# Kernel tuning notes

Hardware: AMD Instinct MI355X
Metric: run time of the kernel (lower is better)

The kernel has to match this reference:

```python
import jax, jax.numpy as jnp
import numpy as np

B = 4096
N = 4097  # num_samples; basis fit uses N-1 columns


def _trapz_cumsum(x, t):
    # y[..., 0] = 0; y[..., i] = y[..., i-1] + 0.5*(t[i]-t[i-1])*(x[..., i-1]+x[..., i])
    dt = t[1:] - t[:-1]                                   # (N-1,)
    inc = 0.5 * dt * (x[..., :-1] + x[..., 1:])           # (B,1,N-1)
    zero = jnp.zeros(x.shape[:-1] + (1,), x.dtype)
    return jnp.concatenate([zero, jnp.cumsum(inc, axis=-1)], axis=-1)  # (B,1,N)


def setup_inputs() -> dict:
    key = jax.random.key(0)
    k1, k2 = jax.random.split(key)
    # positive signal so ny + cumsum(x) stays > 0 (needed for pow/log)
    x = jax.random.uniform(k1, (B, 1, N), dtype=jnp.float32, minval=0.1, maxval=1.1)
    # strictly increasing time grid
    dt = jax.random.uniform(k2, (N,), dtype=jnp.float32, minval=1e-3, maxval=1e-2)
    t = jnp.cumsum(dt)
    params = jnp.array([0.5, 1.0], dtype=jnp.float32)  # [r, ny]
    return {"x": x, "t": t, "params": params}


def reference(x, t, params):
    r, ny = params[0], params[1]
    y = _trapz_cumsum(x, t)                  # (B,1,N)
    z = ny + y[:, 0, 1:]                     # (B,N-1)
    phi = jnp.stack([z, z ** r], axis=1)     # (B,2,N-1)  basis matrix
    phip = jnp.linalg.pinv(phi)              # (B,N-1,2)
    x_sl = x[:, :, 1:]                       # (B,1,N-1)
    coeffs = x_sl @ phip                     # (B,1,2)
    x_hat = coeffs @ phi                     # (B,1,N-1)
    res = x_sl - x_hat                       # (B,1,N-1)
    r2 = jnp.sum(res ** 2, axis=-1)          # (B,1)
    return coeffs, x_hat, res, r2
```

## Files before the change

### kernel.cpp

```cpp
#include <hip/hip_runtime.h>

typedef float f32x4 __attribute__((ext_vector_type(4)));

constexpr int NPTS = 4097;
constexpr int M    = 4096;
constexpr int TPB  = 256;
constexpr int NW   = TPB / 64;
constexpr int NJ   = 4;

struct Lds {
    float wt[NW][NJ];
    float gram[NW][5];
    float r2s[NW];
};

template<int S>
__device__ __forceinline__ void scan4(const f32x4 a, const f32x4 c,
                                      float d0, float d1, float d2, float d3,
                                      float (&xsj)[4], float (&zlj)[4], float& gsj)
{
    const float m[8] = {a.x, a.y, a.z, a.w, c.x, c.y, c.z, c.w};
    const float x0 = m[S+0], x1 = m[S+1], x2 = m[S+2], x3 = m[S+3], x4 = m[S+4];
    const float i0 = d0 * (x0 + x1);
    const float i1 = d1 * (x1 + x2);
    const float i2 = d2 * (x2 + x3);
    const float i3 = d3 * (x3 + x4);
    zlj[0] = i0;
    zlj[1] = i0 + i1;
    zlj[2] = zlj[1] + i2;
    zlj[3] = zlj[2] + i3;
    gsj = zlj[3];
    xsj[0] = x1; xsj[1] = x2; xsj[2] = x3; xsj[3] = x4;
}

template<int S, bool RHALF>
__device__ __forceinline__ void body(const float* __restrict__ x,
                                     const float* __restrict__ t,
                                     float r, float ny,
                                     float* __restrict__ out,
                                     int b, int B, Lds& L)
{
    const int tid  = threadIdx.x;
    const int lane = tid & 63;
    const int wid  = tid >> 6;

    const float* __restrict__ xal = x + (size_t)b * NPTS - S;

    float xs[NJ][4];
    float zl[NJ][4];
    float gs[NJ];

#pragma unroll
    for (int j = 0; j < NJ; ++j) {
        const int e = j * 1024 + tid * 4;
        const f32x4 a4 = *(const f32x4*)(xal + e);
        const f32x4 c4 = *(const f32x4*)(xal + e + 4);
        const f32x4 tq = *(const f32x4*)(t + e);
        float tn = __shfl_down(tq.x, 1, 64);
        if (lane == 63) tn = t[e + 4];
        const float d0 = 0.5f * (tq.y - tq.x);
        const float d1 = 0.5f * (tq.z - tq.y);
        const float d2 = 0.5f * (tq.w - tq.z);
        const float d3 = 0.5f * (tn   - tq.w);
        scan4<S>(a4, c4, d0, d1, d2, d3, xs[j], zl[j], gs[j]);
    }

    float sc[NJ];
#pragma unroll
    for (int c = 0; c < NJ; ++c) sc[c] = gs[c];
#pragma unroll
    for (int d = 1; d < 64; d <<= 1) {
#pragma unroll
        for (int c = 0; c < NJ; ++c) {
            float u = __shfl_up(sc[c], d, 64);
            if (lane >= d) sc[c] += u;
        }
    }
    if (lane == 63) {
#pragma unroll
        for (int c = 0; c < NJ; ++c) L.wt[wid][c] = sc[c];
    }
    __syncthreads();

    float woff[NJ] = {}, Tt[NJ] = {};
#pragma unroll
    for (int w = 0; w < NW; ++w) {
#pragma unroll
        for (int c = 0; c < NJ; ++c) {
            const float v = L.wt[w][c];
            Tt[c] += v;
            if (w < wid) woff[c] += v;
        }
    }
    float zb[NJ];
    {
        float jacc = 0.f;
#pragma unroll
        for (int j = 0; j < NJ; ++j) {
            zb[j] = ny + jacc + woff[j] + (sc[j] - gs[j]);
            jacc += Tt[j];
        }
    }

    float s0 = 0, s1 = 0, s2 = 0, s3 = 0, s4 = 0;
#pragma unroll
    for (int j = 0; j < NJ; ++j) {
        float pzz = 0, pzw = 0, pww = 0, pxz = 0, pxw = 0;
#pragma unroll
        for (int i = 0; i < 4; ++i) {
            const float z = zb[j] + zl[j][i];
            zl[j][i] = z;
            const float w = RHALF ? sqrtf(z) : powf(z, r);
            const float xv = xs[j][i];
            pzz = fmaf(z,  z, pzz);
            pzw = fmaf(z,  w, pzw);
            pww = fmaf(w,  w, pww);
            pxz = fmaf(xv, z, pxz);
            pxw = fmaf(xv, w, pxw);
        }
        s0 += pzz; s1 += pzw; s2 += pww; s3 += pxz; s4 += pxw;
    }
#pragma unroll
    for (int d = 32; d > 0; d >>= 1) {
        s0 += __shfl_down(s0, d, 64);
        s1 += __shfl_down(s1, d, 64);
        s2 += __shfl_down(s2, d, 64);
        s3 += __shfl_down(s3, d, 64);
        s4 += __shfl_down(s4, d, 64);
    }
    if (lane == 0) {
        L.gram[wid][0] = s0; L.gram[wid][1] = s1; L.gram[wid][2] = s2;
        L.gram[wid][3] = s3; L.gram[wid][4] = s4;
    }
    __syncthreads();

    double a0 = 0, a1 = 0, a2 = 0, a3 = 0, a4 = 0;
#pragma unroll
    for (int w = 0; w < NW; ++w) {
        a0 += L.gram[w][0]; a1 += L.gram[w][1]; a2 += L.gram[w][2];
        a3 += L.gram[w][3]; a4 += L.gram[w][4];
    }
    const double det = a0 * a2 - a1 * a1;
    const double inv = 1.0 / det;
    const float c0 = (float)((a3 * a2 - a4 * a1) * inv);
    const float c1 = (float)((a4 * a0 - a3 * a1) * inv);
    if (tid == 0) {
        out[(size_t)b * 2 + 0] = c0;
        out[(size_t)b * 2 + 1] = c1;
    }

    float* __restrict__ xhat = out + (size_t)B * 2 + (size_t)b * M;
    float* __restrict__ res  = xhat + (size_t)B * M;

    float r2 = 0.f;
#pragma unroll
    for (int j = 0; j < NJ; ++j) {
        const int e = j * 1024 + tid * 4;
        f32x4 hv, rv;
#pragma unroll
        for (int i = 0; i < 4; ++i) {
            const float z = zl[j][i];
            const float w = RHALF ? sqrtf(z) : powf(z, r);
            const float h  = c0 * z + c1 * w;
            const float ev = xs[j][i] - h;
            hv[i] = h; rv[i] = ev;
            r2 = fmaf(ev, ev, r2);
        }
        *(f32x4*)(xhat + e) = hv;
        *(f32x4*)(res  + e) = rv;
    }
#pragma unroll
    for (int d = 32; d > 0; d >>= 1) r2 += __shfl_down(r2, d, 64);
    if (lane == 0) L.r2s[wid] = r2;
    __syncthreads();
    if (tid == 0) {
        float acc = 0.f;
#pragma unroll
        for (int w = 0; w < NW; ++w) acc += L.r2s[w];
        out[(size_t)B * 2 + 2 * (size_t)B * M + b] = acc;
    }
}

__global__ __launch_bounds__(TPB)
void vp_kernel(const float* __restrict__ x, const float* __restrict__ t,
               const float* __restrict__ params, float* __restrict__ out, int B)
{
    __shared__ Lds L;
    const float r  = params[0];
    const float ny = params[1];
    const int  b   = blockIdx.x;

    if (r == 0.5f) {
        switch (b & 3) {
        case 0:  body<0, true>(x, t, r, ny, out, b, B, L); break;
        case 1:  body<1, true>(x, t, r, ny, out, b, B, L); break;
        case 2:  body<2, true>(x, t, r, ny, out, b, B, L); break;
        default: body<3, true>(x, t, r, ny, out, b, B, L); break;
        }
    } else {
        switch (b & 3) {
        case 0:  body<0, false>(x, t, r, ny, out, b, B, L); break;
        case 1:  body<1, false>(x, t, r, ny, out, b, B, L); break;
        case 2:  body<2, false>(x, t, r, ny, out, b, B, L); break;
        default: body<3, false>(x, t, r, ny, out, b, B, L); break;
        }
    }
}

extern "C" void kernel_launch(void* const* d_in, const int* in_sizes, int n_in,
                              void* d_out, int out_size, void* d_ws, size_t ws_size,
                              hipStream_t stream) {
    const float* x = (const float*)d_in[0];
    const float* t = (const float*)d_in[1];
    const float* p = (const float*)d_in[2];
    float* out     = (float*)d_out;
    const int B    = in_sizes[0] / NPTS;

    vp_kernel<<<dim3(B), dim3(TPB), 0, stream>>>(x, t, p, out, B);
}
```

Measured before the change: 41.29 us.

## Map one row per wavefront and recompute scan from global memory per pass

Each wavefront now processes a whole row instead of a 256-thread block per row, which removes all LDS traffic and block barriers. Rows are handled in 16 sequential chunks with a wave-level prefix scan that carries a running sum. Only the per-chunk base offsets are kept in registers; x and t are re-read from memory and the local scan is recomputed in the Gram and output passes. This trades extra loads (mostly cache hits) and a serial per-chunk scan for lower register pressure and more resident waves via launch_bounds occupancy 8. Grid size assumes B is divisible by 4.

Measured after the change: 70.03 us. +69.6%, slower.

```diff
diff --git a/kernel.cpp b/kernel.cpp
--- a/kernel.cpp
+++ b/kernel.cpp
@@ -5,113 +5,80 @@
 constexpr int NPTS = 4097;
 constexpr int M    = 4096;
 constexpr int TPB  = 256;
-constexpr int NW   = TPB / 64;
-constexpr int NJ   = 4;
-
-struct Lds {
-    float wt[NW][NJ];
-    float gram[NW][5];
-    float r2s[NW];
-};
+constexpr int WPB  = 4;
+constexpr int NG   = 16;
 
 template<int S>
-__device__ __forceinline__ void scan4(const f32x4 a, const f32x4 c,
-                                      float d0, float d1, float d2, float d3,
-                                      float (&xsj)[4], float (&zlj)[4], float& gsj)
+__device__ __forceinline__ void group_u(const f32x4 a, const f32x4 c,
+                                        const f32x4 tq, float tn,
+                                        float (&u)[4], float (&xsj)[4])
 {
     const float m[8] = {a.x, a.y, a.z, a.w, c.x, c.y, c.z, c.w};
     const float x0 = m[S+0], x1 = m[S+1], x2 = m[S+2], x3 = m[S+3], x4 = m[S+4];
+    const float d0 = 0.5f * (tq.y - tq.x);
+    const float d1 = 0.5f * (tq.z - tq.y);
+    const float d2 = 0.5f * (tq.w - tq.z);
+    const float d3 = 0.5f * (tn   - tq.w);
     const float i0 = d0 * (x0 + x1);
     const float i1 = d1 * (x1 + x2);
     const float i2 = d2 * (x2 + x3);
     const float i3 = d3 * (x3 + x4);
-    zlj[0] = i0;
-    zlj[1] = i0 + i1;
-    zlj[2] = zlj[1] + i2;
-    zlj[3] = zlj[2] + i3;
-    gsj = zlj[3];
+    u[0] = i0;
+    u[1] = i0 + i1;
+    u[2] = u[1] + i2;
+    u[3] = u[2] + i3;
     xsj[0] = x1; xsj[1] = x2; xsj[2] = x3; xsj[3] = x4;
 }
 
 template<int S, bool RHALF>
-__device__ __forceinline__ void body(const float* __restrict__ x,
-                                     const float* __restrict__ t,
-                                     float r, float ny,
-                                     float* __restrict__ out,
-                                     int b, int B, Lds& L)
+__device__ __forceinline__ void wave_body(
+    const float* __restrict__ x, const float* __restrict__ t,
+    float r, float ny, float* __restrict__ out, int b, int B)
 {
-    const int tid  = threadIdx.x;
-    const int lane = tid & 63;
-    const int wid  = tid >> 6;
-
+    const int lane = threadIdx.x & 63;
     const float* __restrict__ xal = x + (size_t)b * NPTS - S;
 
-    float xs[NJ][4];
-    float zl[NJ][4];
-    float gs[NJ];
-
-#pragma unroll
-    for (int j = 0; j < NJ; ++j) {
-        const int e = j * 1024 + tid * 4;
-        const f32x4 a4 = *(const f32x4*)(xal + e);
-        const f32x4 c4 = *(const f32x4*)(xal + e + 4);
-        const f32x4 tq = *(const f32x4*)(t + e);
-        float tn = __shfl_down(tq.x, 1, 64);
-        if (lane == 63) tn = t[e + 4];
-        const float d0 = 0.5f * (tq.y - tq.x);
-        const float d1 = 0.5f * (tq.z - tq.y);
-        const float d2 = 0.5f * (tq.w - tq.z);
-        const float d3 = 0.5f * (tn   - tq.w);
-        scan4<S>(a4, c4, d0, d1, d2, d3, xs[j], zl[j], gs[j]);
-    }
-
-    float sc[NJ];
-#pragma unroll
-    for (int c = 0; c < NJ; ++c) sc[c] = gs[c];
-#pragma unroll
-    for (int d = 1; d < 64; d <<= 1) {
-#pragma unroll
-        for (int c = 0; c < NJ; ++c) {
-            float u = __shfl_up(sc[c], d, 64);
-            if (lane >= d) sc[c] += u;
-        }
-    }
-    if (lane == 63) {
-#pragma unroll
-        for (int c = 0; c < NJ; ++c) L.wt[wid][c] = sc[c];
-    }
-    __syncthreads();
-
-    float woff[NJ] = {}, Tt[NJ] = {};
-#pragma unroll
-    for (int w = 0; w < NW; ++w) {
-#pragma unroll
-        for (int c = 0; c < NJ; ++c) {
-            const float v = L.wt[w][c];
-            Tt[c] += v;
-            if (w < wid) woff[c] += v;
-        }
-    }
-    float zb[NJ];
+    float zbb[NG];
     {
         float jacc = 0.f;
+#pragma unroll 4
+        for (int j = 0; j < NG; ++j) {
+            const int e = j * 256 + lane * 4;
+            const f32x4 a  = *(const f32x4*)(xal + e);
+            const f32x4 c  = *(const f32x4*)(xal + e + 4);
+            const f32x4 tq = *(const f32x4*)(t + e);
+            float tn = __shfl_down(tq.x, 1, 64);
+            if (lane == 63) tn = t[e + 4];
+            float u[4], xsj[4];
+            group_u<S>(a, c, tq, tn, u, xsj);
+            float inc = u[3];
 #pragma unroll
-        for (int j = 0; j < NJ; ++j) {
-            zb[j] = ny + jacc + woff[j] + (sc[j] - gs[j]);
-            jacc += Tt[j];
+            for (int d = 1; d < 64; d <<= 1) {
+                float v = __shfl_up(inc, d, 64);
+                if (lane >= d) inc += v;
+            }
+            zbb[j] = ny + jacc + (inc - u[3]);
+            jacc += __shfl(inc, 63, 64);
         }
     }
 
     float s0 = 0, s1 = 0, s2 = 0, s3 = 0, s4 = 0;
-#pragma unroll
-    for (int j = 0; j < NJ; ++j) {
+#pragma unroll 4
+    for (int j = 0; j < NG; ++j) {
+        const int e = j * 256 + lane * 4;
+        const f32x4 a  = *(const f32x4*)(xal + e);
+        const f32x4 c  = *(const f32x4*)(xal + e + 4);
+        const f32x4 tq = *(const f32x4*)(t + e);
+        float tn = __shfl_down(tq.x, 1, 64);
+        if (lane == 63) tn = t[e + 4];
+        float u[4], xsj[4];
+        group_u<S>(a, c, tq, tn, u, xsj);
         float pzz = 0, pzw = 0, pww = 0, pxz = 0, pxw = 0;
 #pragma unroll
         for (int i = 0; i < 4; ++i) {
-            const float z = zb[j] + zl[j][i];
-            zl[j][i] = z;
-            const float w = RHALF ? sqrtf(z) : powf(z, r);
-            const float xv = xs[j][i];
+            const float z  = zbb[j] + u[i];
+            const float w  = RHALF ? sqrtf(z) : powf(z, r);
+            const float xv = xsj[i];
             pzz = fmaf(z,  z, pzz);
             pzw = fmaf(z,  w, pzw);
             pww = fmaf(w,  w, pww);
@@ -121,30 +88,20 @@
         s0 += pzz; s1 += pzw; s2 += pww; s3 += pxz; s4 += pxw;
     }
 #pragma unroll
-    for (int d = 32; d > 0; d >>= 1) {
-        s0 += __shfl_down(s0, d, 64);
-        s1 += __shfl_down(s1, d, 64);
-        s2 += __shfl_down(s2, d, 64);
-        s3 += __shfl_down(s3, d, 64);
-        s4 += __shfl_down(s4, d, 64);
+    for (int mq = 1; mq < 64; mq <<= 1) {
+        s0 += __shfl_xor(s0, mq, 64);
+        s1 += __shfl_xor(s1, mq, 64);
+        s2 += __shfl_xor(s2, mq, 64);
+        s3 += __shfl_xor(s3, mq, 64);
+        s4 += __shfl_xor(s4, mq, 64);
     }
-    if (lane == 0) {
-        L.gram[wid][0] = s0; L.gram[wid][1] = s1; L.gram[wid][2] = s2;
-        L.gram[wid][3] = s3; L.gram[wid][4] = s4;
-    }
-    __syncthreads();
 
-    double a0 = 0, a1 = 0, a2 = 0, a3 = 0, a4 = 0;
-#pragma unroll
-    for (int w = 0; w < NW; ++w) {
-        a0 += L.gram[w][0]; a1 += L.gram[w][1]; a2 += L.gram[w][2];
-        a3 += L.gram[w][3]; a4 += L.gram[w][4];
-    }
+    const double a0 = s0, a1 = s1, a2 = s2, a3 = s3, a4 = s4;
     const double det = a0 * a2 - a1 * a1;
     const double inv = 1.0 / det;
     const float c0 = (float)((a3 * a2 - a4 * a1) * inv);
     const float c1 = (float)((a4 * a0 - a3 * a1) * inv);
-    if (tid == 0) {
+    if (lane == 0) {
         out[(size_t)b * 2 + 0] = c0;
         out[(size_t)b * 2 + 1] = c1;
     }
@@ -153,56 +110,59 @@
     float* __restrict__ res  = xhat + (size_t)B * M;
 
     float r2 = 0.f;
-#pragma unroll
-    for (int j = 0; j < NJ; ++j) {
-        const int e = j * 1024 + tid * 4;
+#pragma unroll 4
+    for (int j = 0; j < NG; ++j) {
+        const int e = j * 256 + lane * 4;
+        const f32x4 a  = *(const f32x4*)(xal + e);
+        const f32x4 c  = *(const f32x4*)(xal + e + 4);
+        const f32x4 tq = *(const f32x4*)(t + e);
+        float tn = __shfl_down(tq.x, 1, 64);
+        if (lane == 63) tn = t[e + 4];
+        float u[4], xsj[4];
+        group_u<S>(a, c, tq, tn, u, xsj);
         f32x4 hv, rv;
+        float p = 0.f;
 #pragma unroll
         for (int i = 0; i < 4; ++i) {
-            const float z = zl[j][i];
-            const float w = RHALF ? sqrtf(z) : powf(z, r);
+            const float z  = zbb[j] + u[i];
+            const float w  = RHALF ? sqrtf(z) : powf(z, r);
             const float h  = c0 * z + c1 * w;
-            const float ev = xs[j][i] - h;
+            const float ev = xsj[i] - h;
             hv[i] = h; rv[i] = ev;
-            r2 = fmaf(ev, ev, r2);
+            p = fmaf(ev, ev, p);
         }
         *(f32x4*)(xhat + e) = hv;
         *(f32x4*)(res  + e) = rv;
+        r2 += p;
     }
 #pragma unroll
-    for (int d = 32; d > 0; d >>= 1) r2 += __shfl_down(r2, d, 64);
-    if (lane == 0) L.r2s[wid] = r2;
-    __syncthreads();
-    if (tid == 0) {
-        float acc = 0.f;
-#pragma unroll
-        for (int w = 0; w < NW; ++w) acc += L.r2s[w];
-        out[(size_t)B * 2 + 2 * (size_t)B * M + b] = acc;
-    }
+    for (int mq = 1; mq < 64; mq <<= 1) r2 += __shfl_xor(r2, mq, 64);
+    if (lane == 0)
+        out[(size_t)B * 2 + 2 * (size_t)B * M + b] = r2;
 }
 
-__global__ __launch_bounds__(TPB)
+__global__ __launch_bounds__(TPB, 8)
 void vp_kernel(const float* __restrict__ x, const float* __restrict__ t,
                const float* __restrict__ params, float* __restrict__ out, int B)
 {
-    __shared__ Lds L;
-    const float r  = params[0];
-    const float ny = params[1];
-    const int  b   = blockIdx.x;
+    const float r   = params[0];
+    const float ny  = params[1];
+    const int   wid = threadIdx.x >> 6;
+    const int   b   = blockIdx.x * WPB + wid;
 
     if (r == 0.5f) {
-        switch (b & 3) {
-        case 0:  body<0, true>(x, t, r, ny, out, b, B, L); break;
-        case 1:  body<1, true>(x, t, r, ny, out, b, B, L); break;
-        case 2:  body<2, true>(x, t, r, ny, out, b, B, L); break;
-        default: body<3, true>(x, t, r, ny, out, b, B, L); break;
+        switch (wid) {
+        case 0:  wave_body<0, true>(x, t, r, ny, out, b, B); break;
+        case 1:  wave_body<1, true>(x, t, r, ny, out, b, B); break;
+        case 2:  wave_body<2, true>(x, t, r, ny, out, b, B); break;
+        default: wave_body<3, true>(x, t, r, ny, out, b, B); break;
         }
     } else {
-        switch (b & 3) {
-        case 0:  body<0, false>(x, t, r, ny, out, b, B, L); break;
-        case 1:  body<1, false>(x, t, r, ny, out, b, B, L); break;
-        case 2:  body<2, false>(x, t, r, ny, out, b, B, L); break;
-        default: body<3, false>(x, t, r, ny, out, b, B, L); break;
+        switch (wid) {
+        case 0:  wave_body<0, false>(x, t, r, ny, out, b, B); break;
+        case 1:  wave_body<1, false>(x, t, r, ny, out, b, B); break;
+        case 2:  wave_body<2, false>(x, t, r, ny, out, b, B); break;
+        default: wave_body<3, false>(x, t, r, ny, out, b, B); break;
         }
     }
 }
@@ -216,5 +176,5 @@
     float* out     = (float*)d_out;
     const int B    = in_sizes[0] / NPTS;
 
-    vp_kernel<<<dim3(B), dim3(TPB), 0, stream>>>(x, t, p, out, B);
+    vp_kernel<<<dim3(B / WPB), dim3(TPB), 0, stream>>>(x, t, p, out, B);
 }
```
